# Kernel optimization log

Measured on AMD Instinct MI355X. Metric: run time of the kernel, lower is better.

The kernel has to match this reference:

```python
import jax, jax.numpy as jnp
import numpy as np

D_MODEL = 64

def setup_inputs() -> dict:
    key = jax.random.key(0)
    k1, k2, k3, k4, k5, k6 = jax.random.split(key, 6)
    b, h, t, s, d = 2, 8, 384, 384, D_MODEL
    scale = 1.0 / np.sqrt(d)
    return {
        "query": jax.random.normal(k1, (b, h, t, d), dtype=jnp.float32),
        "key": jax.random.normal(k2, (b, h, s, d), dtype=jnp.float32),
        "value": jax.random.normal(k3, (b, h, s, d), dtype=jnp.float32),
        # torch nn.Linear(d,d,bias=False) weight W: y = x @ W.T; store W as (out,in)
        "Wq": jax.random.uniform(k4, (d, d), jnp.float32, -scale, scale),
        "Wk": jax.random.uniform(k5, (d, d), jnp.float32, -scale, scale),
        # v: Linear(d,1) -> weight shape (1,d); store as vector (d,)
        "v_w": jax.random.uniform(k6, (d,), jnp.float32, -scale, scale),
    }

def reference(query, key, value, Wq, Wk, v_w):
    # Linearity lets us project BEFORE broadcasting (same math as projecting
    # the (b,h,t,s,d) expanded tensors, far less FLOPs/memory for the GEMMs).
    qp = jnp.einsum('bhtd,ed->bhte', query, Wq)   # W_q * q
    kp = jnp.einsum('bhsd,ed->bhse', key, Wk)     # W_k * k
    # combined: (b,h,t,s,d) broadcast add + tanh (the big intermediate)
    combined = jnp.tanh(qp[:, :, :, None, :] + kp[:, :, None, :, :])
    score = jnp.einsum('bhtsd,d->bhts', combined, v_w)  # v^T tanh(...)
    attn_weights = jax.nn.softmax(score, axis=-1)        # (b,h,t,s)
    out = jnp.einsum('bhts,bhsd->bhtd', attn_weights, value)
    return (out, attn_weights)
```

## Files before the change

kernel.cpp:

```cpp
#include <hip/hip_runtime.h>
#include <hip/hip_bf16.h>

#define BH 16
#define NT 384
#define NS 384
#define DD 64

static constexpr float TWO_LOG2E = 2.8853900817779268f;
static constexpr float LOG2E     = 1.4426950408889634f;

__device__ float4 g_Ea4[(size_t)BH * NT * DD / 4];
__device__ float4 g_Eb4[(size_t)BH * NS * DD / 4];
__device__ float4 g_part4[2 * (size_t)BH * NT * DD / 4];

__global__ __launch_bounds__(256) void k1_proj(
    const float* __restrict__ q, const float* __restrict__ k,
    const float* __restrict__ Wq, const float* __restrict__ Wk)
{
    __shared__ float xt[32 * 64];
    const int bid    = blockIdx.x;
    const int tensor = bid / 192;
    const int tile   = bid % 192;
    const int tid  = threadIdx.x;
    const int lane = tid & 63;
    const int w    = tid >> 6;

    const float* __restrict__ X = tensor ? k  : q;
    const float* __restrict__ W = tensor ? Wk : Wq;
    float* __restrict__ E = tensor ? (float*)g_Eb4 : (float*)g_Ea4;

    const size_t base = (size_t)tile * 32;

    {
        const float4* __restrict__ src =
            reinterpret_cast<const float4*>(X + base * 64);
        float4* dst = reinterpret_cast<float4*>(xt);
#pragma unroll
        for (int i = 0; i < 2; ++i) dst[tid + i * 256] = src[tid + i * 256];
    }

    float wr[64];
    {
        const float* wrow = W + lane * 64;
#pragma unroll
        for (int i = 0; i < 64; i += 4) {
            float4 v = *reinterpret_cast<const float4*>(wrow + i);
            wr[i] = v.x; wr[i + 1] = v.y; wr[i + 2] = v.z; wr[i + 3] = v.w;
        }
    }
    __syncthreads();

#pragma unroll
    for (int r8 = 0; r8 < 8; ++r8) {
        const int r = w * 8 + r8;
        float a0 = 0.f, a1 = 0.f, a2 = 0.f, a3 = 0.f;
#pragma unroll
        for (int d4 = 0; d4 < 16; ++d4) {
            const float4 xv = *reinterpret_cast<const float4*>(&xt[r * 64 + d4 * 4]);
            a0 = fmaf(xv.x, wr[d4 * 4 + 0], a0);
            a1 = fmaf(xv.y, wr[d4 * 4 + 1], a1);
            a2 = fmaf(xv.z, wr[d4 * 4 + 2], a2);
            a3 = fmaf(xv.w, wr[d4 * 4 + 3], a3);
        }
        const float dot = (a0 + a1) + (a2 + a3);
        E[(base + r) * 64 + lane] = __builtin_amdgcn_exp2f(TWO_LOG2E * dot);
    }
}

__global__ __launch_bounds__(256) void k2_scores(
    const float* __restrict__ v_w, float* __restrict__ attn)
{
    __shared__ float ea[32 * 64];
    __shared__ float ebl[64 * 68];
    const int bid = blockIdx.x;
    const int bh  = bid / 72;
    const int rem = bid % 72;
    const int tt  = rem / 6;
    const int sc  = rem % 6;
    const int tid  = threadIdx.x;
    const int lane = tid & 63;
    const int w    = tid >> 6;

    const float* Ea = (const float*)g_Ea4;
    const float* Eb = (const float*)g_Eb4;

    {
        const float4* __restrict__ src =
            reinterpret_cast<const float4*>(Ea + ((size_t)bh * NT + tt * 32) * 64);
        float4* dst = reinterpret_cast<float4*>(ea);
#pragma unroll
        for (int i = 0; i < 2; ++i) dst[tid + i * 256] = src[tid + i * 256];
    }
    {
        const float4* __restrict__ src =
            reinterpret_cast<const float4*>(Eb + ((size_t)bh * NS + sc * 64) * 64);
#pragma unroll
        for (int i = 0; i < 4; ++i) {
            const int j   = tid + i * 256;
            const int row = j >> 4;
            const int c4  = j & 15;
            *reinterpret_cast<float4*>(&ebl[row * 68 + c4 * 4]) = src[j];
        }
    }

    float vv[64];
#pragma unroll
    for (int i = 0; i < 64; i += 4) {
        float4 v = *reinterpret_cast<const float4*>(v_w + i);
        vv[i] = v.x; vv[i + 1] = v.y; vv[i + 2] = v.z; vv[i + 3] = v.w;
    }
    float C0 = 0.f;
#pragma unroll
    for (int i = 0; i < 64; ++i) C0 += vv[i];

    __syncthreads();

    float eb[64];
#pragma unroll
    for (int e4 = 0; e4 < 16; ++e4) {
        float4 v = *reinterpret_cast<const float4*>(&ebl[lane * 68 + e4 * 4]);
        eb[e4 * 4 + 0] = v.x; eb[e4 * 4 + 1] = v.y;
        eb[e4 * 4 + 2] = v.z; eb[e4 * 4 + 3] = v.w;
    }

#pragma unroll
    for (int r8 = 0; r8 < 8; ++r8) {
        const int tloc = w * 8 + r8;
        float a0 = 0.f, a1 = 0.f, a2 = 0.f, a3 = 0.f;
#pragma unroll
        for (int e4 = 0; e4 < 16; ++e4) {
            const float4 A = *reinterpret_cast<const float4*>(&ea[tloc * 64 + e4 * 4]);
            const float d0 = fmaf(A.x, eb[e4 * 4 + 0], 1.0f);
            const float d1 = fmaf(A.y, eb[e4 * 4 + 1], 1.0f);
            const float d2 = fmaf(A.z, eb[e4 * 4 + 2], 1.0f);
            const float d3 = fmaf(A.w, eb[e4 * 4 + 3], 1.0f);
            a0 = fmaf(vv[e4 * 4 + 0], __builtin_amdgcn_rcpf(d0), a0);
            a1 = fmaf(vv[e4 * 4 + 1], __builtin_amdgcn_rcpf(d1), a1);
            a2 = fmaf(vv[e4 * 4 + 2], __builtin_amdgcn_rcpf(d2), a2);
            a3 = fmaf(vv[e4 * 4 + 3], __builtin_amdgcn_rcpf(d3), a3);
        }
        const float score = C0 - 2.0f * ((a0 + a1) + (a2 + a3));
        attn[((size_t)bh * NT + tt * 32 + tloc) * NS + sc * 64 + lane] = score;
    }
}

__global__ __launch_bounds__(256) void k3_softmax(float* __restrict__ attn)
{
    const int row  = blockIdx.x * 4 + (threadIdx.x >> 6);
    const int lane = threadIdx.x & 63;

    float* __restrict__ sr = attn + (size_t)row * NS;
    float v0 = sr[lane];
    float v1 = sr[lane + 64];
    float v2 = sr[lane + 128];
    float v3 = sr[lane + 192];
    float v4 = sr[lane + 256];
    float v5 = sr[lane + 320];
    float m = fmaxf(fmaxf(fmaxf(v0, v1), fmaxf(v2, v3)), fmaxf(v4, v5));
#pragma unroll
    for (int o = 32; o > 0; o >>= 1) m = fmaxf(m, __shfl_xor(m, o, 64));
    const float p0 = __builtin_amdgcn_exp2f((v0 - m) * LOG2E);
    const float p1 = __builtin_amdgcn_exp2f((v1 - m) * LOG2E);
    const float p2 = __builtin_amdgcn_exp2f((v2 - m) * LOG2E);
    const float p3 = __builtin_amdgcn_exp2f((v3 - m) * LOG2E);
    const float p4 = __builtin_amdgcn_exp2f((v4 - m) * LOG2E);
    const float p5 = __builtin_amdgcn_exp2f((v5 - m) * LOG2E);
    float s = ((p0 + p1) + (p2 + p3)) + (p4 + p5);
#pragma unroll
    for (int o = 32; o > 0; o >>= 1) s += __shfl_xor(s, o, 64);
    const float inv = __builtin_amdgcn_rcpf(s);
    sr[lane]       = p0 * inv;
    sr[lane + 64]  = p1 * inv;
    sr[lane + 128] = p2 * inv;
    sr[lane + 192] = p3 * inv;
    sr[lane + 256] = p4 * inv;
    sr[lane + 320] = p5 * inv;
}

__global__ __launch_bounds__(256) void k4_pv(
    const float* __restrict__ attn, const float* __restrict__ V)
{
    __shared__ float vt[64 * 64];
    __shared__ float at[16 * 64];
    const int bid = blockIdx.x;
    const int bh  = bid / 48;
    const int rem = bid % 48;
    const int tt  = rem / 2;
    const int sh  = rem % 2;
    const int tid  = threadIdx.x;
    const int lane = tid & 63;
    const int w    = tid >> 6;

    float acc[4] = {0.f, 0.f, 0.f, 0.f};

    for (int sc3 = 0; sc3 < 3; ++sc3) {
        const int sc = sh * 3 + sc3;
        __syncthreads();
        {
            const float4* __restrict__ src =
                reinterpret_cast<const float4*>(V + ((size_t)bh * NS + sc * 64) * 64);
            float4* dst = reinterpret_cast<float4*>(vt);
#pragma unroll
            for (int i = 0; i < 4; ++i) dst[tid + i * 256] = src[tid + i * 256];
        }
        {
            const int row = tid >> 4;
            const int c4  = tid & 15;
            const float4* __restrict__ src = reinterpret_cast<const float4*>(
                attn + ((size_t)bh * NT + tt * 16 + row) * NS + sc * 64);
            *reinterpret_cast<float4*>(&at[row * 64 + c4 * 4]) = src[c4];
        }
        __syncthreads();

        float vr[64];
#pragma unroll
        for (int i = 0; i < 64; ++i) vr[i] = vt[i * 64 + lane];

#pragma unroll
        for (int t4 = 0; t4 < 4; ++t4) {
            const int tloc = w * 4 + t4;
            float p0 = 0.f, p1 = 0.f, p2 = 0.f, p3 = 0.f;
#pragma unroll
            for (int e4 = 0; e4 < 16; ++e4) {
                const float4 P = *reinterpret_cast<const float4*>(&at[tloc * 64 + e4 * 4]);
                p0 = fmaf(P.x, vr[e4 * 4 + 0], p0);
                p1 = fmaf(P.y, vr[e4 * 4 + 1], p1);
                p2 = fmaf(P.z, vr[e4 * 4 + 2], p2);
                p3 = fmaf(P.w, vr[e4 * 4 + 3], p3);
            }
            acc[t4] += (p0 + p1) + (p2 + p3);
        }
    }

    float* __restrict__ part = (float*)g_part4 + (size_t)sh * BH * NT * DD;
#pragma unroll
    for (int t4 = 0; t4 < 4; ++t4) {
        const int t = tt * 16 + w * 4 + t4;
        part[((size_t)bh * NT + t) * DD + lane] = acc[t4];
    }
}

__global__ __launch_bounds__(256) void k5_combine(float4* __restrict__ out4)
{
    const int i = blockIdx.x * 256 + threadIdx.x;
    const float4 a = g_part4[i];
    const float4 b = g_part4[i + (size_t)BH * NT * DD / 4];
    float4 r;
    r.x = a.x + b.x; r.y = a.y + b.y; r.z = a.z + b.z; r.w = a.w + b.w;
    out4[i] = r;
}

extern "C" void kernel_launch(void* const* d_in, const int* in_sizes, int n_in,
                              void* d_out, int out_size, void* d_ws, size_t ws_size,
                              hipStream_t stream) {
    const float* q  = (const float*)d_in[0];
    const float* k  = (const float*)d_in[1];
    const float* v  = (const float*)d_in[2];
    const float* Wq = (const float*)d_in[3];
    const float* Wk = (const float*)d_in[4];
    const float* vw = (const float*)d_in[5];

    float* out  = (float*)d_out;
    float* attn = out + (size_t)BH * NT * DD;

    k1_proj   <<<384,  256, 0, stream>>>(q, k, Wq, Wk);
    k2_scores <<<1152, 256, 0, stream>>>(vw, attn);
    k3_softmax<<<1536, 256, 0, stream>>>(attn);
    k4_pv     <<<768,  256, 0, stream>>>(attn, v);
    k5_combine<<<384,  256, 0, stream>>>((float4*)out);
}
```

Before: 118.8 us.

## Fuse scores, softmax and PV into one kernel with whole rows per wave

Result: slower. 122.7 us (+3.3%).

```diff
diff --git a/kernel.cpp b/kernel.cpp
--- a/kernel.cpp
+++ b/kernel.cpp
@@ -11,7 +11,6 @@
 
 __device__ float4 g_Ea4[(size_t)BH * NT * DD / 4];
 __device__ float4 g_Eb4[(size_t)BH * NS * DD / 4];
-__device__ float4 g_part4[2 * (size_t)BH * NT * DD / 4];
 
 __global__ __launch_bounds__(256) void k1_proj(
     const float* __restrict__ q, const float* __restrict__ k,
@@ -67,187 +66,150 @@
     }
 }
 
-__global__ __launch_bounds__(256) void k2_scores(
-    const float* __restrict__ v_w, float* __restrict__ attn)
+__global__ __launch_bounds__(256) void k2_fused(
+    const float* __restrict__ v_w, const float* __restrict__ V,
+    float* __restrict__ out, float* __restrict__ attn)
 {
-    __shared__ float ea[32 * 64];
-    __shared__ float ebl[64 * 68];
-    const int bid = blockIdx.x;
-    const int bh  = bid / 72;
-    const int rem = bid % 72;
-    const int tt  = rem / 6;
-    const int sc  = rem % 6;
+    __shared__ float stage[64 * 68];
+
+    const int bid  = blockIdx.x;
+    const int bh   = bid / 48;
+    const int t0   = (bid % 48) * 8;
     const int tid  = threadIdx.x;
     const int lane = tid & 63;
-    const int w    = tid >> 6;
-
-    const float* Ea = (const float*)g_Ea4;
-    const float* Eb = (const float*)g_Eb4;
-
-    {
-        const float4* __restrict__ src =
-            reinterpret_cast<const float4*>(Ea + ((size_t)bh * NT + tt * 32) * 64);
-        float4* dst = reinterpret_cast<float4*>(ea);
-#pragma unroll
-        for (int i = 0; i < 2; ++i) dst[tid + i * 256] = src[tid + i * 256];
-    }
-    {
-        const float4* __restrict__ src =
-            reinterpret_cast<const float4*>(Eb + ((size_t)bh * NS + sc * 64) * 64);
-#pragma unroll
-        for (int i = 0; i < 4; ++i) {
-            const int j   = tid + i * 256;
-            const int row = j >> 4;
-            const int c4  = j & 15;
-            *reinterpret_cast<float4*>(&ebl[row * 68 + c4 * 4]) = src[j];
-        }
-    }
-
-    float vv[64];
-#pragma unroll
-    for (int i = 0; i < 64; i += 4) {
-        float4 v = *reinterpret_cast<const float4*>(v_w + i);
-        vv[i] = v.x; vv[i + 1] = v.y; vv[i + 2] = v.z; vv[i + 3] = v.w;
-    }
+    const int wv   = __builtin_amdgcn_readfirstlane(tid >> 6);
+    const int r0   = t0 + 2 * wv;
+
     float C0 = 0.f;
 #pragma unroll
-    for (int i = 0; i < 64; ++i) C0 += vv[i];
-
-    __syncthreads();
-
-    float eb[64];
-#pragma unroll
-    for (int e4 = 0; e4 < 16; ++e4) {
-        float4 v = *reinterpret_cast<const float4*>(&ebl[lane * 68 + e4 * 4]);
-        eb[e4 * 4 + 0] = v.x; eb[e4 * 4 + 1] = v.y;
-        eb[e4 * 4 + 2] = v.z; eb[e4 * 4 + 3] = v.w;
-    }
-
-#pragma unroll
-    for (int r8 = 0; r8 < 8; ++r8) {
-        const int tloc = w * 8 + r8;
-        float a0 = 0.f, a1 = 0.f, a2 = 0.f, a3 = 0.f;
-#pragma unroll
-        for (int e4 = 0; e4 < 16; ++e4) {
-            const float4 A = *reinterpret_cast<const float4*>(&ea[tloc * 64 + e4 * 4]);
-            const float d0 = fmaf(A.x, eb[e4 * 4 + 0], 1.0f);
-            const float d1 = fmaf(A.y, eb[e4 * 4 + 1], 1.0f);
-            const float d2 = fmaf(A.z, eb[e4 * 4 + 2], 1.0f);
-            const float d3 = fmaf(A.w, eb[e4 * 4 + 3], 1.0f);
-            a0 = fmaf(vv[e4 * 4 + 0], __builtin_amdgcn_rcpf(d0), a0);
-            a1 = fmaf(vv[e4 * 4 + 1], __builtin_amdgcn_rcpf(d1), a1);
-            a2 = fmaf(vv[e4 * 4 + 2], __builtin_amdgcn_rcpf(d2), a2);
-            a3 = fmaf(vv[e4 * 4 + 3], __builtin_amdgcn_rcpf(d3), a3);
-        }
-        const float score = C0 - 2.0f * ((a0 + a1) + (a2 + a3));
-        attn[((size_t)bh * NT + tt * 32 + tloc) * NS + sc * 64 + lane] = score;
-    }
-}
-
-__global__ __launch_bounds__(256) void k3_softmax(float* __restrict__ attn)
-{
-    const int row  = blockIdx.x * 4 + (threadIdx.x >> 6);
-    const int lane = threadIdx.x & 63;
-
-    float* __restrict__ sr = attn + (size_t)row * NS;
-    float v0 = sr[lane];
-    float v1 = sr[lane + 64];
-    float v2 = sr[lane + 128];
-    float v3 = sr[lane + 192];
-    float v4 = sr[lane + 256];
-    float v5 = sr[lane + 320];
-    float m = fmaxf(fmaxf(fmaxf(v0, v1), fmaxf(v2, v3)), fmaxf(v4, v5));
-#pragma unroll
-    for (int o = 32; o > 0; o >>= 1) m = fmaxf(m, __shfl_xor(m, o, 64));
-    const float p0 = __builtin_amdgcn_exp2f((v0 - m) * LOG2E);
-    const float p1 = __builtin_amdgcn_exp2f((v1 - m) * LOG2E);
-    const float p2 = __builtin_amdgcn_exp2f((v2 - m) * LOG2E);
-    const float p3 = __builtin_amdgcn_exp2f((v3 - m) * LOG2E);
-    const float p4 = __builtin_amdgcn_exp2f((v4 - m) * LOG2E);
-    const float p5 = __builtin_amdgcn_exp2f((v5 - m) * LOG2E);
-    float s = ((p0 + p1) + (p2 + p3)) + (p4 + p5);
-#pragma unroll
-    for (int o = 32; o > 0; o >>= 1) s += __shfl_xor(s, o, 64);
-    const float inv = __builtin_amdgcn_rcpf(s);
-    sr[lane]       = p0 * inv;
-    sr[lane + 64]  = p1 * inv;
-    sr[lane + 128] = p2 * inv;
-    sr[lane + 192] = p3 * inv;
-    sr[lane + 256] = p4 * inv;
-    sr[lane + 320] = p5 * inv;
-}
-
-__global__ __launch_bounds__(256) void k4_pv(
-    const float* __restrict__ attn, const float* __restrict__ V)
-{
-    __shared__ float vt[64 * 64];
-    __shared__ float at[16 * 64];
-    const int bid = blockIdx.x;
-    const int bh  = bid / 48;
-    const int rem = bid % 48;
-    const int tt  = rem / 2;
-    const int sh  = rem % 2;
-    const int tid  = threadIdx.x;
-    const int lane = tid & 63;
-    const int w    = tid >> 6;
-
-    float acc[4] = {0.f, 0.f, 0.f, 0.f};
-
-    for (int sc3 = 0; sc3 < 3; ++sc3) {
-        const int sc = sh * 3 + sc3;
+    for (int i = 0; i < 64; ++i) C0 += v_w[i];
+
+    const float* __restrict__ ea0 = (const float*)g_Ea4 + ((size_t)bh * NT + r0) * 64;
+    const float* __restrict__ ea1 = ea0 + 64;
+    const float* __restrict__ Eb  = (const float*)g_Eb4 + (size_t)bh * NS * 64;
+
+    float p0[6], p1[6];
+
+    for (int sc = 0; sc < 6; ++sc) {
         __syncthreads();
         {
             const float4* __restrict__ src =
-                reinterpret_cast<const float4*>(V + ((size_t)bh * NS + sc * 64) * 64);
-            float4* dst = reinterpret_cast<float4*>(vt);
-#pragma unroll
-            for (int i = 0; i < 4; ++i) dst[tid + i * 256] = src[tid + i * 256];
-        }
+                reinterpret_cast<const float4*>(Eb + (size_t)sc * 64 * 64);
+#pragma unroll
+            for (int i = 0; i < 4; ++i) {
+                const int j = tid + i * 256;
+                const float4 v = src[j];
+                const int s  = j >> 4;
+                const int e4 = j & 15;
+                stage[(e4 * 4 + 0) * 65 + s] = v.x;
+                stage[(e4 * 4 + 1) * 65 + s] = v.y;
+                stage[(e4 * 4 + 2) * 65 + s] = v.z;
+                stage[(e4 * 4 + 3) * 65 + s] = v.w;
+            }
+        }
+        __syncthreads();
+
+        float a00 = 0.f, a01 = 0.f, a02 = 0.f, a03 = 0.f;
+        float a10 = 0.f, a11 = 0.f, a12 = 0.f, a13 = 0.f;
+#pragma unroll
+        for (int e = 0; e < 64; e += 4) {
+            const float b0 = stage[(e + 0) * 65 + lane];
+            const float b1 = stage[(e + 1) * 65 + lane];
+            const float b2 = stage[(e + 2) * 65 + lane];
+            const float b3 = stage[(e + 3) * 65 + lane];
+            a00 = fmaf(v_w[e + 0], __builtin_amdgcn_rcpf(fmaf(ea0[e + 0], b0, 1.f)), a00);
+            a01 = fmaf(v_w[e + 1], __builtin_amdgcn_rcpf(fmaf(ea0[e + 1], b1, 1.f)), a01);
+            a02 = fmaf(v_w[e + 2], __builtin_amdgcn_rcpf(fmaf(ea0[e + 2], b2, 1.f)), a02);
+            a03 = fmaf(v_w[e + 3], __builtin_amdgcn_rcpf(fmaf(ea0[e + 3], b3, 1.f)), a03);
+            a10 = fmaf(v_w[e + 0], __builtin_amdgcn_rcpf(fmaf(ea1[e + 0], b0, 1.f)), a10);
+            a11 = fmaf(v_w[e + 1], __builtin_amdgcn_rcpf(fmaf(ea1[e + 1], b1, 1.f)), a11);
+            a12 = fmaf(v_w[e + 2], __builtin_amdgcn_rcpf(fmaf(ea1[e + 2], b2, 1.f)), a12);
+            a13 = fmaf(v_w[e + 3], __builtin_amdgcn_rcpf(fmaf(ea1[e + 3], b3, 1.f)), a13);
+        }
+        p0[sc] = C0 - 2.f * ((a00 + a01) + (a02 + a03));
+        p1[sc] = C0 - 2.f * ((a10 + a11) + (a12 + a13));
+    }
+
+    {
+        float m0 = fmaxf(fmaxf(fmaxf(p0[0], p0[1]), fmaxf(p0[2], p0[3])), fmaxf(p0[4], p0[5]));
+        float m1 = fmaxf(fmaxf(fmaxf(p1[0], p1[1]), fmaxf(p1[2], p1[3])), fmaxf(p1[4], p1[5]));
+#pragma unroll
+        for (int o = 32; o > 0; o >>= 1) {
+            m0 = fmaxf(m0, __shfl_xor(m0, o, 64));
+            m1 = fmaxf(m1, __shfl_xor(m1, o, 64));
+        }
+        float s0 = 0.f, s1 = 0.f;
+#pragma unroll
+        for (int i = 0; i < 6; ++i) {
+            p0[i] = __builtin_amdgcn_exp2f((p0[i] - m0) * LOG2E);
+            p1[i] = __builtin_amdgcn_exp2f((p1[i] - m1) * LOG2E);
+            s0 += p0[i];
+            s1 += p1[i];
+        }
+#pragma unroll
+        for (int o = 32; o > 0; o >>= 1) {
+            s0 += __shfl_xor(s0, o, 64);
+            s1 += __shfl_xor(s1, o, 64);
+        }
+        const float i0 = __builtin_amdgcn_rcpf(s0);
+        const float i1 = __builtin_amdgcn_rcpf(s1);
+        float* __restrict__ ar0 = attn + ((size_t)bh * NT + r0) * NS;
+        float* __restrict__ ar1 = ar0 + NS;
+#pragma unroll
+        for (int i = 0; i < 6; ++i) {
+            p0[i] *= i0;
+            p1[i] *= i1;
+            ar0[i * 64 + lane] = p0[i];
+            ar1[i * 64 + lane] = p1[i];
+        }
+    }
+
+    const int g  = lane >> 4;
+    const int d4 = (lane & 15) * 4;
+    float4 O0 = {0.f, 0.f, 0.f, 0.f};
+    float4 O1 = {0.f, 0.f, 0.f, 0.f};
+    const float4* __restrict__ Vg =
+        reinterpret_cast<const float4*>(V + (size_t)bh * NS * 64);
+
+    for (int sc = 0; sc < 6; ++sc) {
+        __syncthreads();
         {
-            const int row = tid >> 4;
-            const int c4  = tid & 15;
-            const float4* __restrict__ src = reinterpret_cast<const float4*>(
-                attn + ((size_t)bh * NT + tt * 16 + row) * NS + sc * 64);
-            *reinterpret_cast<float4*>(&at[row * 64 + c4 * 4]) = src[c4];
-        }
-        __syncthreads();
-
-        float vr[64];
-#pragma unroll
-        for (int i = 0; i < 64; ++i) vr[i] = vt[i * 64 + lane];
-
-#pragma unroll
-        for (int t4 = 0; t4 < 4; ++t4) {
-            const int tloc = w * 4 + t4;
-            float p0 = 0.f, p1 = 0.f, p2 = 0.f, p3 = 0.f;
-#pragma unroll
-            for (int e4 = 0; e4 < 16; ++e4) {
-                const float4 P = *reinterpret_cast<const float4*>(&at[tloc * 64 + e4 * 4]);
-                p0 = fmaf(P.x, vr[e4 * 4 + 0], p0);
-                p1 = fmaf(P.y, vr[e4 * 4 + 1], p1);
-                p2 = fmaf(P.z, vr[e4 * 4 + 2], p2);
-                p3 = fmaf(P.w, vr[e4 * 4 + 3], p3);
+#pragma unroll
+            for (int i = 0; i < 4; ++i) {
+                const int j = tid + i * 256;
+                const float4 v = Vg[(size_t)sc * 1024 + j];
+                const int row = j >> 4;
+                const int c4  = j & 15;
+                *reinterpret_cast<float4*>(&stage[row * 68 + c4 * 4]) = v;
             }
-            acc[t4] += (p0 + p1) + (p2 + p3);
-        }
-    }
-
-    float* __restrict__ part = (float*)g_part4 + (size_t)sh * BH * NT * DD;
-#pragma unroll
-    for (int t4 = 0; t4 < 4; ++t4) {
-        const int t = tt * 16 + w * 4 + t4;
-        part[((size_t)bh * NT + t) * DD + lane] = acc[t4];
-    }
-}
-
-__global__ __launch_bounds__(256) void k5_combine(float4* __restrict__ out4)
-{
-    const int i = blockIdx.x * 256 + threadIdx.x;
-    const float4 a = g_part4[i];
-    const float4 b = g_part4[i + (size_t)BH * NT * DD / 4];
-    float4 r;
-    r.x = a.x + b.x; r.y = a.y + b.y; r.z = a.z + b.z; r.w = a.w + b.w;
-    out4[i] = r;
+        }
+        __syncthreads();
+
+#pragma unroll
+        for (int s4 = 0; s4 < 16; ++s4) {
+            const int sl = s4 * 4 + g;
+            const float4 v4 = *reinterpret_cast<const float4*>(&stage[sl * 68 + d4]);
+            const float q0 = __shfl(p0[sc], sl, 64);
+            const float q1 = __shfl(p1[sc], sl, 64);
+            O0.x = fmaf(q0, v4.x, O0.x); O0.y = fmaf(q0, v4.y, O0.y);
+            O0.z = fmaf(q0, v4.z, O0.z); O0.w = fmaf(q0, v4.w, O0.w);
+            O1.x = fmaf(q1, v4.x, O1.x); O1.y = fmaf(q1, v4.y, O1.y);
+            O1.z = fmaf(q1, v4.z, O1.z); O1.w = fmaf(q1, v4.w, O1.w);
+        }
+    }
+
+#pragma unroll
+    for (int o = 16; o <= 32; o <<= 1) {
+        O0.x += __shfl_xor(O0.x, o, 64); O0.y += __shfl_xor(O0.y, o, 64);
+        O0.z += __shfl_xor(O0.z, o, 64); O0.w += __shfl_xor(O0.w, o, 64);
+        O1.x += __shfl_xor(O1.x, o, 64); O1.y += __shfl_xor(O1.y, o, 64);
+        O1.z += __shfl_xor(O1.z, o, 64); O1.w += __shfl_xor(O1.w, o, 64);
+    }
+    if (g == 0) {
+        float* __restrict__ op = out + ((size_t)bh * NT + r0) * 64 + d4;
+        *reinterpret_cast<float4*>(op)      = O0;
+        *reinterpret_cast<float4*>(op + 64) = O1;
+    }
 }
 
 extern "C" void kernel_launch(void* const* d_in, const int* in_sizes, int n_in,
@@ -263,9 +225,6 @@
     float* out  = (float*)d_out;
     float* attn = out + (size_t)BH * NT * DD;
 
-    k1_proj   <<<384,  256, 0, stream>>>(q, k, Wq, Wk);
-    k2_scores <<<1152, 256, 0, stream>>>(vw, attn);
-    k3_softmax<<<1536, 256, 0, stream>>>(attn);
-    k4_pv     <<<768,  256, 0, stream>>>(attn, v);
-    k5_combine<<<384,  256, 0, stream>>>((float4*)out);
+    k1_proj <<<384, 256, 0, stream>>>(q, k, Wq, Wk);
+    k2_fused<<<768, 256, 0, stream>>>(vw, v, out, attn);
 }
```
